# Performance work log

Measured on AMD Instinct MI355X. Metric: run time of the kernel, lower is better.

The kernel has to match this reference:

```python
import jax, jax.numpy as jnp
import numpy as np

E = 1024   # embedding_size
H = 16     # num_heads
DH = E // H


def setup_inputs() -> dict:
    key = jax.random.key(0)
    ks = jax.random.split(key, 11)
    B, S = 2, 2048
    std = 0.02
    return {
        "query": jax.random.normal(ks[0], (B, S, E), jnp.float32),
        "key": jax.random.normal(ks[1], (B, S, E), jnp.float32),
        "value": jax.random.normal(ks[2], (B, S, E), jnp.float32),
        "Wq": jax.random.normal(ks[3], (E, E), jnp.float32) * std,
        "bq": jnp.zeros((E,), jnp.float32),
        "Wk": jax.random.normal(ks[4], (E, E), jnp.float32) * std,
        "bk": jnp.zeros((E,), jnp.float32),
        "Wv": jax.random.normal(ks[5], (E, E), jnp.float32) * std,
        "bv": jnp.zeros((E,), jnp.float32),
        "Wo": jax.random.normal(ks[6], (E, E), jnp.float32) * std,
        "bo": jnp.zeros((E,), jnp.float32),
    }


def _split_heads(x, B, S):
    # [B,S,E] -> [B,H,S,DH]
    return x.reshape(B, S, H, DH).transpose(0, 2, 1, 3)


def reference(query, key, value, Wq, bq, Wk, bk, Wv, bv, Wo, bo):
    B, S, _ = query.shape
    # torch Linear: y = x @ W.T + b
    q = _split_heads(query @ Wq.T + bq, B, S)
    k = _split_heads(key @ Wk.T + bk, B, key.shape[1])
    v = _split_heads(value @ Wv.T + bv, B, value.shape[1])
    # naive unscaled attention (original has no 1/sqrt(d) factor)
    scores = jnp.einsum("bhsd,bhtd->bhst", q, k)  # [B,H,S,T]
    attn = jax.nn.softmax(scores, axis=-1)
    out = jnp.einsum("bhst,bhtd->bhsd", attn, v)  # [B,H,S,DH]
    out = out.transpose(0, 2, 1, 3).reshape(B, S, E)
    return out @ Wo.T + bo
```

## Files before the change

### kernel.cpp

```cpp
#include <hip/hip_runtime.h>
#include <hip/hip_bf16.h>

constexpr int kB   = 2;
constexpr int kS   = 2048;
constexpr int kE   = 1024;
constexpr int kH   = 16;
constexpr int kDH  = 64;
constexpr int kTok = kB * kS;

typedef short bf16x8 __attribute__((ext_vector_type(8)));
typedef float f32x4  __attribute__((ext_vector_type(4)));
typedef unsigned int uint2v __attribute__((ext_vector_type(2)));

__device__ __forceinline__ float bf2f(unsigned short s) {
  union { unsigned int u; float f; } c; c.u = ((unsigned int)s) << 16; return c.f;
}
__device__ __forceinline__ unsigned short f2bf(float f) {
  union { float f; unsigned int u; } c; c.f = f;
  unsigned int u = c.u;
  u += 0x7fffu + ((u >> 16) & 1u);
  return (unsigned short)(u >> 16);
}

__device__ __forceinline__ unsigned cvtpk(float lo, float hi) {
  unsigned r;
  asm("v_cvt_pk_bf16_f32 %0, %1, %2" : "=v"(r) : "v"(lo), "v"(hi));
  return r;
}

__device__ __forceinline__ void gl_lds16(const unsigned short* g, unsigned short* l) {
  __builtin_amdgcn_global_load_lds(
      (const __attribute__((address_space(1))) unsigned int*)g,
      (__attribute__((address_space(3))) unsigned int*)l, 16, 0, 0);
}

__global__ void detect_dtype(const unsigned short* __restrict__ q, int* flag) {
  __shared__ int cnt;
  if (threadIdx.x == 0) cnt = 0;
  __syncthreads();
  int bad = 0;
  for (int i = threadIdx.x; i < 4096; i += 256) {
    unsigned int e = (q[i] >> 7) & 0xFF;
    if (e >= 0xC0) bad++;
  }
  atomicAdd(&cnt, bad);
  __syncthreads();
  if (threadIdx.x == 0) *flag = (cnt > 8) ? 1 : 0;
}

struct Seg { const void* src; unsigned short* dst; unsigned int n; unsigned int blk0; };
struct ConvArgs { Seg s[11]; };

__global__ __launch_bounds__(256) void conv_all(ConvArgs a, const int* __restrict__ flag) {
  const unsigned int bid = blockIdx.x;
  int si = 0;
  #pragma unroll
  for (int i = 1; i < 11; ++i)
    if (bid >= a.s[i].blk0) si = i;
  const Seg sg = a.s[si];
  const int i0 = ((int)(bid - sg.blk0) * 256 + threadIdx.x) * 8;
  if (i0 >= (int)sg.n) return;
  if (*flag) {
    const float* s = (const float*)sg.src + i0;
    f32x4 f0 = *(const f32x4*)(s);
    f32x4 f1 = *(const f32x4*)(s + 4);
    bf16x8 v;
    #pragma unroll
    for (int j = 0; j < 4; ++j) v[j]     = (short)f2bf(f0[j]);
    #pragma unroll
    for (int j = 0; j < 4; ++j) v[j + 4] = (short)f2bf(f1[j]);
    *(bf16x8*)&sg.dst[i0] = v;
  } else {
    *(bf16x8*)&sg.dst[i0] = *(const bf16x8*)((const unsigned short*)sg.src + i0);
  }
}

__device__ __forceinline__ void gemm_core(
    const unsigned short* __restrict__ A,
    const unsigned short* __restrict__ W,
    int Kdim, int bM, int bN,
    unsigned short* As, unsigned short* Ws,
    f32x4 acc[4][4])
{
  const int tid  = threadIdx.x;
  const int lane = tid & 63;
  const int wv   = tid >> 6;
  const int wm   = (wv >> 1) * 64;
  const int wn   = (wv & 1) * 64;
  const int lr   = lane & 15;
  const int kq   = (lane >> 4) * 8;

  const int r0 = tid >> 2;
  const int c0 = (tid & 3) * 8;

  const unsigned short* Ag = A + (size_t)(bM + r0) * Kdim + c0;
  const unsigned short* Wg = W + (size_t)(bN + r0) * Kdim + c0;
  unsigned short* lA = &As[tid * 8];
  unsigned short* lW = &Ws[tid * 8];

  for (int k0 = 0; k0 < Kdim; k0 += 32) {
    gl_lds16(Ag + k0,                      lA);
    gl_lds16(Ag + (size_t)64 * Kdim + k0,  lA + 2048);
    gl_lds16(Wg + k0,                      lW);
    gl_lds16(Wg + (size_t)64 * Kdim + k0,  lW + 2048);
    __syncthreads();

    bf16x8 a[4], b[4];
    #pragma unroll
    for (int i = 0; i < 4; ++i)
      a[i] = *(const bf16x8*)&As[(wm + i * 16 + lr) * 32 + kq];
    #pragma unroll
    for (int i = 0; i < 4; ++i)
      b[i] = *(const bf16x8*)&Ws[(wn + i * 16 + lr) * 32 + kq];
    #pragma unroll
    for (int i = 0; i < 4; ++i)
      #pragma unroll
      for (int j = 0; j < 4; ++j)
        acc[i][j] = __builtin_amdgcn_mfma_f32_16x16x32_bf16(a[i], b[j], acc[i][j], 0, 0, 0);
    __syncthreads();
  }
}

__global__ __launch_bounds__(256) void gemm_qkv(
    const unsigned short* __restrict__ Abase,
    const unsigned short* __restrict__ Wbase,
    const unsigned short* __restrict__ biasbase,
    unsigned short* __restrict__ Cbase)
{
  __shared__ unsigned short As[128 * 32];
  __shared__ unsigned short Ws[128 * 32];

  const int z = blockIdx.z;
  const unsigned short* A    = Abase    + (size_t)z * (kTok * kE);
  const unsigned short* W    = Wbase    + (size_t)z * (kE * kE);
  const unsigned short* bias = biasbase + (size_t)z * kE;
  unsigned short* C          = Cbase    + (size_t)z * (kTok * kE);

  const int bM = blockIdx.y * 128;
  const int bN = blockIdx.x * 128;

  f32x4 acc[4][4] = {};
  gemm_core(A, W, kE, bM, bN, As, Ws, acc);

  const int lane = threadIdx.x & 63;
  const int wv   = threadIdx.x >> 6;
  const int wm   = (wv >> 1) * 64;
  const int wn   = (wv & 1) * 64;
  const int lr   = lane & 15;
  const int qd   = lane >> 4;
  #pragma unroll
  for (int j = 0; j < 4; ++j) {
    const int col = bN + wn + j * 16 + lr;
    const float bb = bf2f(bias[col]);
    #pragma unroll
    for (int i = 0; i < 4; ++i)
      #pragma unroll
      for (int r = 0; r < 4; ++r) {
        const int row = bM + wm + i * 16 + qd * 4 + r;
        C[(size_t)row * kE + col] = f2bf(acc[i][j][r] + bb);
      }
  }
}

__global__ __launch_bounds__(256) void vtrans(
    const unsigned short* __restrict__ Vb,
    unsigned short* __restrict__ Vt)
{
  __shared__ unsigned short Lt[64 * 72];
  const int tid = threadIdx.x;
  const int bh  = blockIdx.y;
  const int b   = bh >> 4;
  const int h   = bh & 15;
  const int hcol = h * kDH;
  const int s0  = blockIdx.x * 64;

  #pragma unroll
  for (int issue = 0; issue < 2; ++issue) {
    int g = issue * 256 + tid;
    int r = g >> 3, c = (g & 7) * 8;
    bf16x8 vv = *(const bf16x8*)&Vb[(size_t)(b * kS + s0 + r) * kE + hcol + c];
    const int swz = ((((r >> 3) ^ (c >> 3)) & 7) << 3) + (r & 7);
    #pragma unroll
    for (int i = 0; i < 8; ++i)
      Lt[(c + i) * 72 + swz] = (unsigned short)vv[i];
  }
  __syncthreads();
  #pragma unroll
  for (int issue = 0; issue < 2; ++issue) {
    int g = issue * 256 + tid;
    int f = g >> 3, tc = (g & 7) * 8;
    const int blk = ((tc >> 3) ^ (f >> 3)) & 7;
    bf16x8 vv = *(const bf16x8*)&Lt[f * 72 + (blk << 3)];
    *(bf16x8*)&Vt[(size_t)b * (kE * kS) + (size_t)(hcol + f) * kS + s0 + tc] = vv;
  }
}

__global__ __launch_bounds__(256) void gemm_out(
    const unsigned short* __restrict__ A,
    const unsigned short* __restrict__ W,
    const unsigned short* __restrict__ bias,
    void* __restrict__ C,
    const int* __restrict__ flag)
{
  __shared__ unsigned short As[128 * 32];
  __shared__ unsigned short Ws[128 * 32];

  const int bM = blockIdx.y * 128;
  const int bN = blockIdx.x * 128;

  f32x4 acc[4][4] = {};
  gemm_core(A, W, kE, bM, bN, As, Ws, acc);

  const int lane = threadIdx.x & 63;
  const int wv   = threadIdx.x >> 6;
  const int wm   = (wv >> 1) * 64;
  const int wn   = (wv & 1) * 64;
  const int lr   = lane & 15;
  const int qd   = lane >> 4;
  if (*flag) {
    float* Cf = (float*)C;
    #pragma unroll
    for (int j = 0; j < 4; ++j) {
      const int col = bN + wn + j * 16 + lr;
      const float bb = bf2f(bias[col]);
      #pragma unroll
      for (int i = 0; i < 4; ++i)
        #pragma unroll
        for (int r = 0; r < 4; ++r) {
          const int row = bM + wm + i * 16 + qd * 4 + r;
          Cf[(size_t)row * kE + col] = acc[i][j][r] + bb;
        }
    }
  } else {
    unsigned short* Cb = (unsigned short*)C;
    #pragma unroll
    for (int j = 0; j < 4; ++j) {
      const int col = bN + wn + j * 16 + lr;
      const float bb = bf2f(bias[col]);
      #pragma unroll
      for (int i = 0; i < 4; ++i)
        #pragma unroll
        for (int r = 0; r < 4; ++r) {
          const int row = bM + wm + i * 16 + qd * 4 + r;
          Cb[(size_t)row * kE + col] = f2bf(acc[i][j][r] + bb);
        }
    }
  }
}

__global__ __launch_bounds__(256) void attn(
    const unsigned short* __restrict__ Qb,
    const unsigned short* __restrict__ Kb,
    const unsigned short* __restrict__ Vt,
    unsigned short* __restrict__ Ob)
{
  __shared__ unsigned short Qs[64 * 72];
  __shared__ unsigned short Ks[64 * 72];
  __shared__ unsigned short Vs[64 * 72];

  const int tid  = threadIdx.x;
  const int lane = tid & 63;
  const int w    = tid >> 6;
  const int lr   = lane & 15;
  const int quad = lane >> 4;
  const int kq   = quad * 8;

  const int bh = blockIdx.y;
  const int b  = bh >> 4;
  const int h  = bh & 15;
  const int q0 = blockIdx.x * 64;

  const size_t rowbase = (size_t)b * kS * kE;
  const int hcol = h * kDH;
  const unsigned short* Vbase = Vt + (size_t)b * (kE * kS) + (size_t)hcol * kS;

  const int r0 = tid >> 3;
  const int c0 = (tid & 7) * 8;

  #pragma unroll
  for (int issue = 0; issue < 2; ++issue) {
    int r = issue * 32 + r0;
    *(bf16x8*)&Qs[r * 72 + c0] =
        *(const bf16x8*)&Qb[rowbase + (size_t)(q0 + r) * kE + hcol + c0];
  }
  __syncthreads();

  const bf16x8 aq0 = *(const bf16x8*)&Qs[(w * 16 + lr) * 72 + 0 + kq];
  const bf16x8 aq1 = *(const bf16x8*)&Qs[(w * 16 + lr) * 72 + 32 + kq];

  f32x4 o[4] = {};
  float l4[4] = {0.f, 0.f, 0.f, 0.f};

  bf16x8 rk0 = *(const bf16x8*)&Kb[rowbase + (size_t)(r0)      * kE + hcol + c0];
  bf16x8 rk1 = *(const bf16x8*)&Kb[rowbase + (size_t)(r0 + 32) * kE + hcol + c0];
  bf16x8 rv0 = *(const bf16x8*)&Vbase[(size_t)(r0)      * kS + c0];
  bf16x8 rv1 = *(const bf16x8*)&Vbase[(size_t)(r0 + 32) * kS + c0];

  for (int t0 = 0; t0 < kS; t0 += 64) {
    __syncthreads();
    *(bf16x8*)&Ks[ r0       * 72 + c0] = rk0;
    *(bf16x8*)&Ks[(r0 + 32) * 72 + c0] = rk1;
    *(bf16x8*)&Vs[ r0       * 72 + c0] = rv0;
    *(bf16x8*)&Vs[(r0 + 32) * 72 + c0] = rv1;
    __syncthreads();

    const int t1 = t0 + 64;
    if (t1 < kS) {
      rk0 = *(const bf16x8*)&Kb[rowbase + (size_t)(t1 + r0)      * kE + hcol + c0];
      rk1 = *(const bf16x8*)&Kb[rowbase + (size_t)(t1 + r0 + 32) * kE + hcol + c0];
      rv0 = *(const bf16x8*)&Vbase[(size_t)(r0)      * kS + t1 + c0];
      rv1 = *(const bf16x8*)&Vbase[(size_t)(r0 + 32) * kS + t1 + c0];
    }

    f32x4 s[4] = {};
    #pragma unroll
    for (int tn = 0; tn < 4; ++tn) {
      const bf16x8 bk0 = *(const bf16x8*)&Ks[(tn * 16 + lr) * 72 + 0 + kq];
      const bf16x8 bk1 = *(const bf16x8*)&Ks[(tn * 16 + lr) * 72 + 32 + kq];
      s[tn] = __builtin_amdgcn_mfma_f32_16x16x32_bf16(bk0, aq0, s[tn], 0, 0, 0);
      s[tn] = __builtin_amdgcn_mfma_f32_16x16x32_bf16(bk1, aq1, s[tn], 0, 0, 0);
    }

    float p[4][4];
    #pragma unroll
    for (int tn = 0; tn < 4; ++tn)
      #pragma unroll
      for (int r = 0; r < 4; ++r) {
        p[tn][r] = __expf(s[tn][r]);
        l4[r] += p[tn][r];
      }

    bf16x8 ap[2];
    #pragma unroll
    for (int kk = 0; kk < 2; ++kk) {
      const unsigned A0 = cvtpk(p[2 * kk][0],     p[2 * kk][1]);
      const unsigned A1 = cvtpk(p[2 * kk + 1][0], p[2 * kk + 1][1]);
      const uint2v u   = __builtin_amdgcn_permlane32_swap(A0, A1, false, false);
      const uint2v z02 = __builtin_amdgcn_permlane16_swap(u[0], u[1], false, false);
      const unsigned B0 = cvtpk(p[2 * kk][2],     p[2 * kk][3]);
      const unsigned B1 = cvtpk(p[2 * kk + 1][2], p[2 * kk + 1][3]);
      const uint2v v2  = __builtin_amdgcn_permlane32_swap(B0, B1, false, false);
      const uint2v z13 = __builtin_amdgcn_permlane16_swap(v2[0], v2[1], false, false);
      union { unsigned ud[4]; bf16x8 v; } pk;
      pk.ud[0] = z02[0];
      pk.ud[1] = z13[0];
      pk.ud[2] = z02[1];
      pk.ud[3] = z13[1];
      ap[kk] = pk.v;
    }

    #pragma unroll
    for (int kk = 0; kk < 2; ++kk)
      #pragma unroll
      for (int dt = 0; dt < 4; ++dt) {
        const bf16x8 bv = *(const bf16x8*)&Vs[(dt * 16 + lr) * 72 + kk * 32 + kq];
        o[dt] = __builtin_amdgcn_mfma_f32_16x16x32_bf16(ap[kk], bv, o[dt], 0, 0, 0);
      }
  }

  float l = (l4[0] + l4[1]) + (l4[2] + l4[3]);
  l += __shfl_xor(l, 16, 64);
  l += __shfl_xor(l, 32, 64);
  float inv[4];
  #pragma unroll
  for (int r = 0; r < 4; ++r)
    inv[r] = 1.0f / __shfl(l, quad * 4 + r, 64);

  #pragma unroll
  for (int dt = 0; dt < 4; ++dt) {
    #pragma unroll
    for (int r = 0; r < 4; ++r) {
      const int row = q0 + w * 16 + quad * 4 + r;
      const int col = hcol + dt * 16 + lr;
      Ob[rowbase + (size_t)row * kE + col] = f2bf(o[dt][r] * inv[r]);
    }
  }
}

extern "C" void kernel_launch(void* const* d_in, const int* in_sizes, int n_in,
                              void* d_out, int out_size, void* d_ws, size_t ws_size,
                              hipStream_t stream) {
  const int nQKV = kTok * kE;
  const int nW   = kE * kE;
  const int nB   = kE;

  char* wsb = (char*)d_ws;
  int* flag = (int*)wsb;
  unsigned short* qc  = (unsigned short*)(wsb + 16);
  unsigned short* kc  = qc  + (size_t)nQKV;
  unsigned short* vc  = kc  + (size_t)nQKV;
  unsigned short* Wqc = vc  + (size_t)nQKV;
  unsigned short* Wkc = Wqc + (size_t)nW;
  unsigned short* Wvc = Wkc + (size_t)nW;
  unsigned short* Woc = Wvc + (size_t)nW;
  unsigned short* bqc = Woc + (size_t)nW;
  unsigned short* bkc = bqc + nB;
  unsigned short* bvc = bkc + nB;
  unsigned short* boc = bvc + nB;
  unsigned short* Qb  = boc + nB;
  unsigned short* Kb  = Qb  + (size_t)nQKV;
  unsigned short* Vb  = Kb  + (size_t)nQKV;
  unsigned short* Vtb = kc;
  unsigned short* Ob  = qc;

  detect_dtype<<<1, 256, 0, stream>>>((const unsigned short*)d_in[0], flag);

  ConvArgs ca;
  const void* srcs[11] = { d_in[0], d_in[1], d_in[2], d_in[3], d_in[4], d_in[5],
                           d_in[6], d_in[7], d_in[8], d_in[9], d_in[10] };
  unsigned short* dsts[11] = { qc, kc, vc, Wqc, bqc, Wkc, bkc, Wvc, bvc, Woc, boc };
  const unsigned int ns[11] = { (unsigned)nQKV, (unsigned)nQKV, (unsigned)nQKV,
                                (unsigned)nW, (unsigned)nB, (unsigned)nW, (unsigned)nB,
                                (unsigned)nW, (unsigned)nB, (unsigned)nW, (unsigned)nB };
  unsigned int blk = 0;
  for (int i = 0; i < 11; ++i) {
    ca.s[i].src = srcs[i]; ca.s[i].dst = dsts[i]; ca.s[i].n = ns[i]; ca.s[i].blk0 = blk;
    blk += (ns[i] + 2047) / 2048;
  }
  conv_all<<<blk, 256, 0, stream>>>(ca, flag);

  dim3 blk256(256);
  dim3 gqkv(kE / 128, kTok / 128, 3);
  gemm_qkv<<<gqkv, blk256, 0, stream>>>(qc, Wqc, bqc, Qb);

  dim3 gvt(kS / 64, kB * kH);
  vtrans<<<gvt, blk256, 0, stream>>>(Vb, Vtb);

  dim3 gattn(kS / 64, kB * kH);
  attn<<<gattn, blk256, 0, stream>>>(Qb, Kb, Vtb, Ob);

  dim3 gout(kE / 128, kTok / 128);
  gemm_out<<<gout, blk256, 0, stream>>>(Ob, Woc, boc, d_out, flag);
}
```

Measured before the change: 273.9 us.

## Process 128 query rows per attention block to reuse K/V tiles

Each warp now computes two 16-row query groups, so a block covers 128 query rows and each K/V tile staged in shared memory feeds twice as many MFMAs. Q fragments are loaded directly from global memory into registers, which drops the Q shared-memory buffer and its barrier. This cuts K/V global and LDS traffic per query row. In exchange it halves the grid size and raises register pressure, which may reduce occupancy and latency hiding.

Result: faster. 267.6 us (-2.3%).

```diff
diff --git a/kernel.cpp b/kernel.cpp
--- a/kernel.cpp
+++ b/kernel.cpp
@@ -254,7 +254,6 @@
     const unsigned short* __restrict__ Vt,
     unsigned short* __restrict__ Ob)
 {
-  __shared__ unsigned short Qs[64 * 72];
   __shared__ unsigned short Ks[64 * 72];
   __shared__ unsigned short Vs[64 * 72];
 
@@ -268,7 +267,7 @@
   const int bh = blockIdx.y;
   const int b  = bh >> 4;
   const int h  = bh & 15;
-  const int q0 = blockIdx.x * 64;
+  const int q0 = blockIdx.x * 128;
 
   const size_t rowbase = (size_t)b * kS * kE;
   const int hcol = h * kDH;
@@ -277,19 +276,16 @@
   const int r0 = tid >> 3;
   const int c0 = (tid & 7) * 8;
 
-  #pragma unroll
-  for (int issue = 0; issue < 2; ++issue) {
-    int r = issue * 32 + r0;
-    *(bf16x8*)&Qs[r * 72 + c0] =
-        *(const bf16x8*)&Qb[rowbase + (size_t)(q0 + r) * kE + hcol + c0];
-  }
-  __syncthreads();
-
-  const bf16x8 aq0 = *(const bf16x8*)&Qs[(w * 16 + lr) * 72 + 0 + kq];
-  const bf16x8 aq1 = *(const bf16x8*)&Qs[(w * 16 + lr) * 72 + 32 + kq];
-
-  f32x4 o[4] = {};
-  float l4[4] = {0.f, 0.f, 0.f, 0.f};
+  bf16x8 aq[2][2];
+  #pragma unroll
+  for (int rg = 0; rg < 2; ++rg)
+    #pragma unroll
+    for (int hh = 0; hh < 2; ++hh)
+      aq[rg][hh] = *(const bf16x8*)
+          &Qb[rowbase + (size_t)(q0 + w * 32 + rg * 16 + lr) * kE + hcol + hh * 32 + kq];
+
+  f32x4 o[2][4] = {};
+  float l4[2][4] = {};
 
   bf16x8 rk0 = *(const bf16x8*)&Kb[rowbase + (size_t)(r0)      * kE + hcol + c0];
   bf16x8 rk1 = *(const bf16x8*)&Kb[rowbase + (size_t)(r0 + 32) * kE + hcol + c0];
@@ -312,67 +308,84 @@
       rv1 = *(const bf16x8*)&Vbase[(size_t)(r0 + 32) * kS + t1 + c0];
     }
 
-    f32x4 s[4] = {};
+    f32x4 s[2][4];
+    #pragma unroll
+    for (int rg = 0; rg < 2; ++rg)
+      #pragma unroll
+      for (int tn = 0; tn < 4; ++tn)
+        s[rg][tn] = f32x4{0.f, 0.f, 0.f, 0.f};
     #pragma unroll
     for (int tn = 0; tn < 4; ++tn) {
       const bf16x8 bk0 = *(const bf16x8*)&Ks[(tn * 16 + lr) * 72 + 0 + kq];
       const bf16x8 bk1 = *(const bf16x8*)&Ks[(tn * 16 + lr) * 72 + 32 + kq];
-      s[tn] = __builtin_amdgcn_mfma_f32_16x16x32_bf16(bk0, aq0, s[tn], 0, 0, 0);
-      s[tn] = __builtin_amdgcn_mfma_f32_16x16x32_bf16(bk1, aq1, s[tn], 0, 0, 0);
+      #pragma unroll
+      for (int rg = 0; rg < 2; ++rg) {
+        s[rg][tn] = __builtin_amdgcn_mfma_f32_16x16x32_bf16(bk0, aq[rg][0], s[rg][tn], 0, 0, 0);
+        s[rg][tn] = __builtin_amdgcn_mfma_f32_16x16x32_bf16(bk1, aq[rg][1], s[rg][tn], 0, 0, 0);
+      }
     }
 
-    float p[4][4];
-    #pragma unroll
-    for (int tn = 0; tn < 4; ++tn)
-      #pragma unroll
-      for (int r = 0; r < 4; ++r) {
-        p[tn][r] = __expf(s[tn][r]);
-        l4[r] += p[tn][r];
+    #pragma unroll
+    for (int rg = 0; rg < 2; ++rg)
+      #pragma unroll
+      for (int tn = 0; tn < 4; ++tn)
+        #pragma unroll
+        for (int r = 0; r < 4; ++r) {
+          const float e = __expf(s[rg][tn][r]);
+          s[rg][tn][r] = e;
+          l4[rg][r] += e;
+        }
+
+    bf16x8 ap[2][2];
+    #pragma unroll
+    for (int rg = 0; rg < 2; ++rg)
+      #pragma unroll
+      for (int kk = 0; kk < 2; ++kk) {
+        const unsigned A0 = cvtpk(s[rg][2 * kk][0],     s[rg][2 * kk][1]);
+        const unsigned A1 = cvtpk(s[rg][2 * kk + 1][0], s[rg][2 * kk + 1][1]);
+        const uint2v u   = __builtin_amdgcn_permlane32_swap(A0, A1, false, false);
+        const uint2v z02 = __builtin_amdgcn_permlane16_swap(u[0], u[1], false, false);
+        const unsigned B0 = cvtpk(s[rg][2 * kk][2],     s[rg][2 * kk][3]);
+        const unsigned B1 = cvtpk(s[rg][2 * kk + 1][2], s[rg][2 * kk + 1][3]);
+        const uint2v v2  = __builtin_amdgcn_permlane32_swap(B0, B1, false, false);
+        const uint2v z13 = __builtin_amdgcn_permlane16_swap(v2[0], v2[1], false, false);
+        union { unsigned ud[4]; bf16x8 v; } pk;
+        pk.ud[0] = z02[0];
+        pk.ud[1] = z13[0];
+        pk.ud[2] = z02[1];
+        pk.ud[3] = z13[1];
+        ap[rg][kk] = pk.v;
       }
-
-    bf16x8 ap[2];
-    #pragma unroll
-    for (int kk = 0; kk < 2; ++kk) {
-      const unsigned A0 = cvtpk(p[2 * kk][0],     p[2 * kk][1]);
-      const unsigned A1 = cvtpk(p[2 * kk + 1][0], p[2 * kk + 1][1]);
-      const uint2v u   = __builtin_amdgcn_permlane32_swap(A0, A1, false, false);
-      const uint2v z02 = __builtin_amdgcn_permlane16_swap(u[0], u[1], false, false);
-      const unsigned B0 = cvtpk(p[2 * kk][2],     p[2 * kk][3]);
-      const unsigned B1 = cvtpk(p[2 * kk + 1][2], p[2 * kk + 1][3]);
-      const uint2v v2  = __builtin_amdgcn_permlane32_swap(B0, B1, false, false);
-      const uint2v z13 = __builtin_amdgcn_permlane16_swap(v2[0], v2[1], false, false);
-      union { unsigned ud[4]; bf16x8 v; } pk;
-      pk.ud[0] = z02[0];
-      pk.ud[1] = z13[0];
-      pk.ud[2] = z02[1];
-      pk.ud[3] = z13[1];
-      ap[kk] = pk.v;
-    }
 
     #pragma unroll
     for (int kk = 0; kk < 2; ++kk)
       #pragma unroll
       for (int dt = 0; dt < 4; ++dt) {
         const bf16x8 bv = *(const bf16x8*)&Vs[(dt * 16 + lr) * 72 + kk * 32 + kq];
-        o[dt] = __builtin_amdgcn_mfma_f32_16x16x32_bf16(ap[kk], bv, o[dt], 0, 0, 0);
+        #pragma unroll
+        for (int rg = 0; rg < 2; ++rg)
+          o[rg][dt] = __builtin_amdgcn_mfma_f32_16x16x32_bf16(ap[rg][kk], bv, o[rg][dt], 0, 0, 0);
       }
   }
 
-  float l = (l4[0] + l4[1]) + (l4[2] + l4[3]);
-  l += __shfl_xor(l, 16, 64);
-  l += __shfl_xor(l, 32, 64);
-  float inv[4];
-  #pragma unroll
-  for (int r = 0; r < 4; ++r)
-    inv[r] = 1.0f / __shfl(l, quad * 4 + r, 64);
-
-  #pragma unroll
-  for (int dt = 0; dt < 4; ++dt) {
-    #pragma unroll
-    for (int r = 0; r < 4; ++r) {
-      const int row = q0 + w * 16 + quad * 4 + r;
-      const int col = hcol + dt * 16 + lr;
-      Ob[rowbase + (size_t)row * kE + col] = f2bf(o[dt][r] * inv[r]);
+  #pragma unroll
+  for (int rg = 0; rg < 2; ++rg) {
+    float l = (l4[rg][0] + l4[rg][1]) + (l4[rg][2] + l4[rg][3]);
+    l += __shfl_xor(l, 16, 64);
+    l += __shfl_xor(l, 32, 64);
+    float inv[4];
+    #pragma unroll
+    for (int r = 0; r < 4; ++r)
+      inv[r] = 1.0f / __shfl(l, quad * 4 + r, 64);
+
+    #pragma unroll
+    for (int dt = 0; dt < 4; ++dt) {
+      #pragma unroll
+      for (int r = 0; r < 4; ++r) {
+        const int row = q0 + w * 32 + rg * 16 + quad * 4 + r;
+        const int col = hcol + dt * 16 + lr;
+        Ob[rowbase + (size_t)row * kE + col] = f2bf(o[rg][dt][r] * inv[r]);
+      }
     }
   }
 }
@@ -426,7 +439,7 @@
   dim3 gvt(kS / 64, kB * kH);
   vtrans<<<gvt, blk256, 0, stream>>>(Vb, Vtb);
 
-  dim3 gattn(kS / 64, kB * kH);
+  dim3 gattn(kS / 128, kB * kH);
   attn<<<gattn, blk256, 0, stream>>>(Qb, Kb, Vtb, Ob);
 
   dim3 gout(kE / 128, kTok / 128);
```
